# Kernel optimization log

Hardware: AMD Instinct MI355X
Metric: run time of the kernel (lower is better)

Reference implementation:

```python
import jax, jax.numpy as jnp
import numpy as np

HEAD_NUM = 8
NEG = 10000.0


def setup_inputs() -> dict:
    key = jax.random.key(0)
    ks = jax.random.split(key, 8)
    B, S, D = 2, 2048, 512
    sc = 1.0 / np.sqrt(D)
    return {
        "x": jax.random.normal(ks[0], (B, S, D), dtype=jnp.float32),
        "mask": jax.random.randint(ks[1], (B, S), 0, 2, dtype=jnp.int32),
        "Wq": jax.random.normal(ks[2], (D, D), dtype=jnp.float32) * sc,
        "bq": jnp.zeros((D,), jnp.float32),
        "Wk": jax.random.normal(ks[3], (D, D), dtype=jnp.float32) * sc,
        "bk": jnp.zeros((D,), jnp.float32),
        "Wv": jax.random.normal(ks[4], (D, D), dtype=jnp.float32) * sc,
        "bv": jnp.zeros((D,), jnp.float32),
        "Wo": jax.random.normal(ks[5], (D, D), dtype=jnp.float32) * sc,
        "bo": jnp.zeros((D,), jnp.float32),
    }


def _split_heads(t, H):
    B, S, D = t.shape
    return t.reshape(B, S, H, D // H).transpose(0, 2, 1, 3)  # [B,H,S,hd]


def reference(x, mask, Wq, bq, Wk, bk, Wv, bv, Wo, bo):
    B, S, D = x.shape
    H = HEAD_NUM
    hd = D // H
    # linear projections + relu activation (as in keras layer)
    q = jax.nn.relu(x @ Wq + bq)
    k = jax.nn.relu(x @ Wk + bk)
    v = jax.nn.relu(x @ Wv + bv)
    q = _split_heads(q, H)
    k = _split_heads(k, H)
    v = _split_heads(v, H)
    # scaled dot-product scores: scale by sqrt(head_dim) (query last dim after split)
    e = jnp.einsum("bhqd,bhkd->bhqk", q, k) / jnp.sqrt(jnp.float32(hd))
    # causal (history_only) additive mask
    idx = jnp.arange(S)
    causal = (idx[None, :] > idx[:, None]).astype(jnp.float32)  # [S,S]
    e = e - NEG * causal[None, None, :, :]
    # key padding mask, additive
    e = e - NEG * (1.0 - mask.astype(jnp.float32))[:, None, None, :]
    # stable softmax (explicit max-subtract as in source)
    a = jax.nn.softmax(e, axis=-1)
    out = jnp.einsum("bhqk,bhkd->bhqd", a, v)  # [B,H,S,hd]
    out = out.transpose(0, 2, 1, 3).reshape(B, S, D)
    # output projection + activation
    return jax.nn.relu(out @ Wo + bo)
```

## Files before the change

### kernel.cpp

```cpp
#include <hip/hip_runtime.h>
#include <hip/hip_bf16.h>

constexpr int Bc = 2, Sc = 2048, Dc = 512, Hc = 8, HDc = 64;
constexpr float NEGC = 10000.0f;
constexpr float SCALEC = 0.125f;
constexpr int Mtot = Bc * Sc;
constexpr size_t HEADMAT = (size_t)Bc * Hc * Sc * HDc;

typedef __attribute__((ext_vector_type(8))) short          short8;
typedef __attribute__((ext_vector_type(8))) unsigned short ushort8;
typedef __attribute__((ext_vector_type(4))) float          f32x4;

static __device__ __forceinline__ unsigned short f32_to_bf16_bits(float f) {
    unsigned int u = __builtin_bit_cast(unsigned int, f);
    unsigned int r = u + 0x7FFFu + ((u >> 16) & 1u);
    return (unsigned short)(r >> 16);
}

__global__ __launch_bounds__(256)
void convert_x(const float* __restrict__ x, unsigned short* __restrict__ Xb, int n)
{
    const int i = (blockIdx.x * 256 + threadIdx.x) * 4;
    if (i >= n) return;
    const float4 v = *(const float4*)(x + i);
    ushort4 o;
    o.x = f32_to_bf16_bits(v.x);
    o.y = f32_to_bf16_bits(v.y);
    o.z = f32_to_bf16_bits(v.z);
    o.w = f32_to_bf16_bits(v.w);
    *(ushort4*)(Xb + i) = o;
}

__global__ __launch_bounds__(256)
void transpose_w(const float* __restrict__ W0, const float* __restrict__ W1,
                 const float* __restrict__ W2, const float* __restrict__ W3,
                 unsigned short* __restrict__ Wt)
{
    __shared__ float T[64][65];
    const int z = blockIdx.z;
    const float* Wp = (z == 0) ? W0 : (z == 1) ? W1 : (z == 2) ? W2 : W3;
    unsigned short* Op = Wt + (size_t)z * 512 * 512;

    const int kt = blockIdx.y * 64, nt = blockIdx.x * 64;
    const int t = threadIdx.x;
    const int r  = t >> 2, c4 = (t & 3) * 16;

    #pragma unroll
    for (int i = 0; i < 4; ++i) {
        const float4 v = *(const float4*)(Wp + (size_t)(kt + r) * 512 + nt + c4 + 4 * i);
        T[r][c4 + 4*i + 0] = v.x;
        T[r][c4 + 4*i + 1] = v.y;
        T[r][c4 + 4*i + 2] = v.z;
        T[r][c4 + 4*i + 3] = v.w;
    }
    __syncthreads();

    const int n = t >> 2, k4 = (t & 3) * 16;
    #pragma unroll
    for (int i = 0; i < 4; ++i) {
        ushort4 o;
        o.x = f32_to_bf16_bits(T[k4 + 4*i + 0][n]);
        o.y = f32_to_bf16_bits(T[k4 + 4*i + 1][n]);
        o.z = f32_to_bf16_bits(T[k4 + 4*i + 2][n]);
        o.w = f32_to_bf16_bits(T[k4 + 4*i + 3][n]);
        *(ushort4*)(Op + (size_t)(nt + n) * 512 + kt + k4 + 4 * i) = o;
    }
}

template<bool HEADOUT>
__global__ __launch_bounds__(256)
void gemm_tile(const unsigned short* __restrict__ Xb,
               const unsigned short* __restrict__ Wt,
               const float* __restrict__ b0, const float* __restrict__ b1,
               const float* __restrict__ b2,
               unsigned short* __restrict__ Hout,
               float* __restrict__ Yf)
{
    __shared__ short As[128 * 32];
    __shared__ short Bs[64 * 32];

    const int lane = threadIdx.x & 63, wave = threadIdx.x >> 6;
    const int c = lane & 15, g = lane >> 4;
    const int wr = wave >> 1, wc = wave & 1;
    const int z = blockIdx.z;
    const unsigned short* Wp = Wt + (size_t)z * 512 * 512;
    const float* bp = (z == 0) ? b0 : (z == 1) ? b1 : b2;
    const int bm = blockIdx.y * 128;
    const int bn = blockIdx.x * 64;

    const int srow = lane >> 2;
    const int scol = (lane & 3) * 8;

    f32x4 acc[4][2] = {};

    for (int k0 = 0; k0 < 512; k0 += 32) {
        __syncthreads();
        #pragma unroll
        for (int i = 0; i < 2; ++i) {
            const int row = (wave * 2 + i) * 16 + srow;
            const short8 v = *(const short8*)(Xb + (size_t)(bm + row) * 512 + k0 + scol);
            *(short8*)(&As[row * 32 + scol]) = v;
        }
        {
            const int row = wave * 16 + srow;
            const short8 v = *(const short8*)(Wp + (size_t)(bn + row) * 512 + k0 + scol);
            *(short8*)(&Bs[row * 32 + scol]) = v;
        }
        __syncthreads();

        short8 a[4], b[2];
        #pragma unroll
        for (int mi = 0; mi < 4; ++mi)
            a[mi] = *(const short8*)(&As[(wr * 64 + mi * 16 + c) * 32 + g * 8]);
        #pragma unroll
        for (int ni = 0; ni < 2; ++ni)
            b[ni] = *(const short8*)(&Bs[(wc * 32 + ni * 16 + c) * 32 + g * 8]);
        #pragma unroll
        for (int mi = 0; mi < 4; ++mi)
            #pragma unroll
            for (int ni = 0; ni < 2; ++ni)
                acc[mi][ni] = __builtin_amdgcn_mfma_f32_16x16x32_bf16(
                    a[mi], b[ni], acc[mi][ni], 0, 0, 0);
    }

    #pragma unroll
    for (int mi = 0; mi < 4; ++mi) {
        #pragma unroll
        for (int ni = 0; ni < 2; ++ni) {
            const int n = bn + wc * 32 + ni * 16 + c;
            const float bias = bp[n];
            float v[4];
            #pragma unroll
            for (int r = 0; r < 4; ++r)
                v[r] = fmaxf(acc[mi][ni][r] + bias, 0.0f);
            const int mbase = bm + wr * 64 + mi * 16 + 4 * g;
            if constexpr (HEADOUT) {
                const int bb = mbase >> 11, ss = mbase & 2047;
                const int hh = n >> 6, hd = n & 63;
                #pragma unroll
                for (int r = 0; r < 4; ++r)
                    Hout[(size_t)z * HEADMAT +
                         (((size_t)(bb * Hc + hh) * Sc + ss + r) * HDc + hd)] =
                        f32_to_bf16_bits(v[r]);
            } else {
                #pragma unroll
                for (int r = 0; r < 4; ++r)
                    Yf[(size_t)(mbase + r) * 512 + n] = v[r];
            }
        }
    }
}

__global__ __launch_bounds__(256)
void attn_mfma(const short* __restrict__ Qh, const short* __restrict__ Kh,
               const short* __restrict__ Vh, const int* __restrict__ mask,
               unsigned short* __restrict__ Ob)
{
    __shared__ __align__(16) char smem[4 * 4608];

    const int lane = threadIdx.x & 63;
    const int wave = threadIdx.x >> 6;
    const int bid = blockIdx.x;
    const int swz = (bid & 7) * 256 + (bid >> 3);
    const int qt  = swz & 127;
    const int h   = (swz >> 7) & 7;
    const int b   = swz >> 10;
    const int q0  = qt * 16;
    const int c   = lane & 15;
    const int g   = lane >> 4;

    short* vst      = (short*)(smem + wave * 4608);
    float* LaccMine = (float*)(smem + wave * 4608);
    float* LmlMine  = (float*)(smem + wave * 4608 + 4352);

    const size_t headoff = (size_t)(b * Hc + h) * Sc * HDc;
    const short* Qp = Qh + headoff;
    const short* Kp = Kh + headoff;
    const short* Vp = Vh + headoff;
    const int* mb = mask + b * Sc;

    int fb = Sc;
    for (int base = 0; base < Sc; base += 64) {
        unsigned long long bal = __ballot(mb[base + lane] != 0);
        if (bal) { fb = base + (__ffsll((unsigned long long)bal) - 1); break; }
    }
    const int kmax = (fb <= q0) ? (q0 + 16) : Sc;
    const int kend = (kmax + 31) & ~31;

    const int nT   = kend >> 5;
    const int tpw  = (nT + 3) >> 2;
    const int kbeg = wave * tpw * 32;
    const int kfin = min(kend, kbeg + tpw * 32);

    const short8 qf0 = *(const short8*)(Qp + (size_t)(q0 + c) * HDc + g * 8);
    const short8 qf1 = *(const short8*)(Qp + (size_t)(q0 + c) * HDc + 32 + g * 8);

    f32x4 acc[4] = {{0.f,0.f,0.f,0.f},{0.f,0.f,0.f,0.f},
                    {0.f,0.f,0.f,0.f},{0.f,0.f,0.f,0.f}};
    float m = -1e30f, l = 0.0f;

    const int vrow = lane >> 1;
    const int vcol = (lane & 1) * 32;

    for (int k0 = kbeg; k0 < kfin; k0 += 32) {
        const short* vsrc = Vp + (size_t)(k0 + vrow) * HDc + vcol;
        const ushort8 vr0 = *(const ushort8*)(vsrc + 0);
        const ushort8 vr1 = *(const ushort8*)(vsrc + 8);
        const ushort8 vr2 = *(const ushort8*)(vsrc + 16);
        const ushort8 vr3 = *(const ushort8*)(vsrc + 24);

        const short8 kf0a = *(const short8*)(Kp + (size_t)(k0 + c) * HDc + g * 8);
        const short8 kf0b = *(const short8*)(Kp + (size_t)(k0 + c) * HDc + 32 + g * 8);
        const short8 kf1a = *(const short8*)(Kp + (size_t)(k0 + 16 + c) * HDc + g * 8);
        const short8 kf1b = *(const short8*)(Kp + (size_t)(k0 + 16 + c) * HDc + 32 + g * 8);

        f32x4 s0 = {0.f, 0.f, 0.f, 0.f};
        f32x4 s1 = {0.f, 0.f, 0.f, 0.f};
        s0 = __builtin_amdgcn_mfma_f32_16x16x32_bf16(kf0a, qf0, s0, 0, 0, 0);
        s0 = __builtin_amdgcn_mfma_f32_16x16x32_bf16(kf0b, qf1, s0, 0, 0, 0);
        s1 = __builtin_amdgcn_mfma_f32_16x16x32_bf16(kf1a, qf0, s1, 0, 0, 0);
        s1 = __builtin_amdgcn_mfma_f32_16x16x32_bf16(kf1b, qf1, s1, 0, 0, 0);

        const int4 mka = *(const int4*)(mb + k0 + 4 * g);
        const int4 mkb = *(const int4*)(mb + k0 + 16 + 4 * g);
        const int mia[4] = {mka.x, mka.y, mka.z, mka.w};
        const int mib[4] = {mkb.x, mkb.y, mkb.z, mkb.w};

        float e[8];
        float tmax = -1e30f;
        #pragma unroll
        for (int r = 0; r < 4; ++r) {
            const int keya = k0 + 4 * g + r;
            float ea = s0[r] * SCALEC;
            if (keya > q0 + c) ea -= NEGC;
            if (mia[r] == 0)   ea -= NEGC;
            e[r] = ea;
            const int keyb = k0 + 16 + 4 * g + r;
            float eb = s1[r] * SCALEC;
            if (keyb > q0 + c) eb -= NEGC;
            if (mib[r] == 0)   eb -= NEGC;
            e[4 + r] = eb;
            tmax = fmaxf(tmax, fmaxf(ea, eb));
        }
        tmax = fmaxf(tmax, __shfl_xor(tmax, 16));
        tmax = fmaxf(tmax, __shfl_xor(tmax, 32));

        if (__any(tmax > m)) {
            const float mnew = fmaxf(m, tmax);
            const float corr = __expf(m - mnew);
            m = mnew;
            l *= corr;
            float cq[4];
            #pragma unroll
            for (int r = 0; r < 4; ++r) cq[r] = __shfl(corr, 4 * g + r);
            #pragma unroll
            for (int t = 0; t < 4; ++t)
                #pragma unroll
                for (int r = 0; r < 4; ++r) acc[t][r] *= cq[r];
        }

        float p[8], ps = 0.f;
        #pragma unroll
        for (int j = 0; j < 8; ++j) { p[j] = __expf(e[j] - m); ps += p[j]; }
        l += ps;

        short8 pf;
        #pragma unroll
        for (int j = 0; j < 8; ++j) pf[j] = (short)f32_to_bf16_bits(p[j]);

        short* vdst = vst + vrow * 72 + vcol;
        *(ushort8*)(vdst + 0)  = vr0;
        *(ushort8*)(vdst + 8)  = vr1;
        *(ushort8*)(vdst + 16) = vr2;
        *(ushort8*)(vdst + 24) = vr3;

        #pragma unroll
        for (int t = 0; t < 4; ++t) {
            short8 vf;
            #pragma unroll
            for (int j = 0; j < 4; ++j) {
                vf[j]     = vst[(4 * g + j) * 72      + t * 16 + c];
                vf[4 + j] = vst[(16 + 4 * g + j) * 72 + t * 16 + c];
            }
            acc[t] = __builtin_amdgcn_mfma_f32_16x16x32_bf16(pf, vf, acc[t], 0, 0, 0);
        }
    }

    l = l + __shfl_xor(l, 16);
    l = l + __shfl_xor(l, 32);

    if (g == 0) { LmlMine[c] = m; LmlMine[16 + c] = l; }
    #pragma unroll
    for (int t = 0; t < 4; ++t)
        #pragma unroll
        for (int r = 0; r < 4; ++r)
            LaccMine[(4 * g + r) * 68 + t * 16 + c] = acc[t][r];
    __syncthreads();

    const int col = wave * 16 + c;
    #pragma unroll
    for (int r = 0; r < 4; ++r) {
        const int row = 4 * g + r;
        float mu[4], lu[4], ou[4];
        #pragma unroll
        for (int u = 0; u < 4; ++u) {
            const float* LaccU = (const float*)(smem + u * 4608);
            const float* LmlU  = (const float*)(smem + u * 4608 + 4352);
            mu[u] = LmlU[row];
            lu[u] = LmlU[16 + row];
            ou[u] = LaccU[row * 68 + col];
        }
        const float M = fmaxf(fmaxf(mu[0], mu[1]), fmaxf(mu[2], mu[3]));
        float L = 0.f, o = 0.f;
        #pragma unroll
        for (int u = 0; u < 4; ++u) {
            const float w = __expf(mu[u] - M);
            L += w * lu[u];
            o += w * ou[u];
        }
        Ob[(size_t)(b * Sc + q0 + row) * Dc + h * HDc + col] =
            f32_to_bf16_bits(o / L);
    }
}

extern "C" void kernel_launch(void* const* d_in, const int* in_sizes, int n_in,
                              void* d_out, int out_size, void* d_ws, size_t ws_size,
                              hipStream_t stream) {
    const float* x  = (const float*)d_in[0];
    const int* mask = (const int*)d_in[1];
    const float* Wq = (const float*)d_in[2];
    const float* bq = (const float*)d_in[3];
    const float* Wk = (const float*)d_in[4];
    const float* bk = (const float*)d_in[5];
    const float* Wv = (const float*)d_in[6];
    const float* bv = (const float*)d_in[7];
    const float* Wo = (const float*)d_in[8];
    const float* bo = (const float*)d_in[9];
    float* out = (float*)d_out;

    unsigned short* Xb = (unsigned short*)d_ws;
    unsigned short* Wt = Xb + (size_t)Mtot * 512;
    unsigned short* Qh = Wt + (size_t)4 * 512 * 512;
    unsigned short* Kh = Qh + HEADMAT;
    unsigned short* Vh = Kh + HEADMAT;
    unsigned short* Ob = Vh + HEADMAT;

    convert_x<<<dim3((Mtot * 512) / 1024), dim3(256), 0, stream>>>(
        x, Xb, Mtot * 512);
    transpose_w<<<dim3(8, 8, 4), dim3(256), 0, stream>>>(Wq, Wk, Wv, Wo, Wt);
    gemm_tile<true><<<dim3(8, Mtot / 128, 3), dim3(256), 0, stream>>>(
        Xb, Wt, bq, bk, bv, Qh, nullptr);
    attn_mfma<<<dim3(2048), dim3(256), 0, stream>>>(
        (const short*)Qh, (const short*)Kh, (const short*)Vh, mask, Ob);
    gemm_tile<false><<<dim3(8, Mtot / 128, 1), dim3(256), 0, stream>>>(
        Ob, Wt + (size_t)3 * 512 * 512, bo, bo, bo, nullptr, out);
}
```

Baseline: 108.6 us.

## Process 32 queries per attention block to reuse K/V tiles, use exp2

The attention kernel now handles two 16-row query tiles per block, so each K and V tile loaded from global memory and staged in LDS feeds twice as many MFMAs. The grid is halved, shared memory per wave doubles, and register use rises with the second set of accumulators. Softmax is rewritten in base 2 with prescaled constants, so exp2 replaces expf. The causal comparison is skipped for key tiles that lie entirely before the query tile. Fewer blocks and higher register pressure may reduce occupancy and latency hiding.

Result: no change. 109.7 us (+1.0%).

```diff
diff --git a/kernel.cpp b/kernel.cpp
--- a/kernel.cpp
+++ b/kernel.cpp
@@ -2,14 +2,16 @@
 #include <hip/hip_bf16.h>
 
 constexpr int Bc = 2, Sc = 2048, Dc = 512, Hc = 8, HDc = 64;
-constexpr float NEGC = 10000.0f;
-constexpr float SCALEC = 0.125f;
 constexpr int Mtot = Bc * Sc;
 constexpr size_t HEADMAT = (size_t)Bc * Hc * Sc * HDc;
+constexpr float SC2  = 0.18033688011112042f;
+constexpr float NEG2 = 14426.950408889634f;
 
 typedef __attribute__((ext_vector_type(8))) short          short8;
 typedef __attribute__((ext_vector_type(8))) unsigned short ushort8;
 typedef __attribute__((ext_vector_type(4))) float          f32x4;
+
+#define MFMA16 __builtin_amdgcn_mfma_f32_16x16x32_bf16
 
 static __device__ __forceinline__ unsigned short f32_to_bf16_bits(float f) {
     unsigned int u = __builtin_bit_cast(unsigned int, f);
@@ -108,19 +110,18 @@
         }
         __syncthreads();
 
-        short8 a[4], b[2];
+        short8 a[4], bfr[2];
         #pragma unroll
         for (int mi = 0; mi < 4; ++mi)
             a[mi] = *(const short8*)(&As[(wr * 64 + mi * 16 + c) * 32 + g * 8]);
         #pragma unroll
         for (int ni = 0; ni < 2; ++ni)
-            b[ni] = *(const short8*)(&Bs[(wc * 32 + ni * 16 + c) * 32 + g * 8]);
+            bfr[ni] = *(const short8*)(&Bs[(wc * 32 + ni * 16 + c) * 32 + g * 8]);
         #pragma unroll
         for (int mi = 0; mi < 4; ++mi)
             #pragma unroll
             for (int ni = 0; ni < 2; ++ni)
-                acc[mi][ni] = __builtin_amdgcn_mfma_f32_16x16x32_bf16(
-                    a[mi], b[ni], acc[mi][ni], 0, 0, 0);
+                acc[mi][ni] = MFMA16(a[mi], bfr[ni], acc[mi][ni], 0, 0, 0);
     }
 
     #pragma unroll
@@ -156,22 +157,23 @@
                const short* __restrict__ Vh, const int* __restrict__ mask,
                unsigned short* __restrict__ Ob)
 {
-    __shared__ __align__(16) char smem[4 * 4608];
+    __shared__ __align__(16) char smem[4 * 9216];
 
     const int lane = threadIdx.x & 63;
     const int wave = threadIdx.x >> 6;
-    const int bid = blockIdx.x;
-    const int swz = (bid & 7) * 256 + (bid >> 3);
-    const int qt  = swz & 127;
-    const int h   = (swz >> 7) & 7;
-    const int b   = swz >> 10;
-    const int q0  = qt * 16;
-    const int c   = lane & 15;
-    const int g   = lane >> 4;
-
-    short* vst      = (short*)(smem + wave * 4608);
-    float* LaccMine = (float*)(smem + wave * 4608);
-    float* LmlMine  = (float*)(smem + wave * 4608 + 4352);
+    const int bid  = blockIdx.x;
+    const int swz  = (bid & 7) * 128 + (bid >> 3);
+    const int qt   = swz & 63;
+    const int h    = (swz >> 6) & 7;
+    const int b    = swz >> 9;
+    const int q0   = qt * 32;
+    const int c    = lane & 15;
+    const int g    = lane >> 4;
+
+    char*  wbase = smem + wave * 9216;
+    short* vst   = (short*)wbase;
+    float* Lacc  = (float*)wbase;
+    float* Lml   = (float*)(wbase + 8704);
 
     const size_t headoff = (size_t)(b * Hc + h) * Sc * HDc;
     const short* Qp = Qh + headoff;
@@ -182,22 +184,23 @@
     int fb = Sc;
     for (int base = 0; base < Sc; base += 64) {
         unsigned long long bal = __ballot(mb[base + lane] != 0);
-        if (bal) { fb = base + (__ffsll((unsigned long long)bal) - 1); break; }
-    }
-    const int kmax = (fb <= q0) ? (q0 + 16) : Sc;
+        if (bal) { fb = base + (__ffsll(bal) - 1); break; }
+    }
+    const int kmax = (fb <= q0) ? (q0 + 32) : Sc;
     const int kend = (kmax + 31) & ~31;
-
     const int nT   = kend >> 5;
     const int tpw  = (nT + 3) >> 2;
     const int kbeg = wave * tpw * 32;
     const int kfin = min(kend, kbeg + tpw * 32);
 
-    const short8 qf0 = *(const short8*)(Qp + (size_t)(q0 + c) * HDc + g * 8);
-    const short8 qf1 = *(const short8*)(Qp + (size_t)(q0 + c) * HDc + 32 + g * 8);
-
-    f32x4 acc[4] = {{0.f,0.f,0.f,0.f},{0.f,0.f,0.f,0.f},
-                    {0.f,0.f,0.f,0.f},{0.f,0.f,0.f,0.f}};
-    float m = -1e30f, l = 0.0f;
+    const short8 qa0 = *(const short8*)(Qp + (size_t)(q0 + c) * HDc + g * 8);
+    const short8 qa1 = *(const short8*)(Qp + (size_t)(q0 + c) * HDc + 32 + g * 8);
+    const short8 qb0 = *(const short8*)(Qp + (size_t)(q0 + 16 + c) * HDc + g * 8);
+    const short8 qb1 = *(const short8*)(Qp + (size_t)(q0 + 16 + c) * HDc + 32 + g * 8);
+
+    f32x4 accA[4] = {{0,0,0,0},{0,0,0,0},{0,0,0,0},{0,0,0,0}};
+    f32x4 accB[4] = {{0,0,0,0},{0,0,0,0},{0,0,0,0},{0,0,0,0}};
+    float mA = -1e30f, lA = 0.f, mB = -1e30f, lB = 0.f;
 
     const int vrow = lane >> 1;
     const int vcol = (lane & 1) * 32;
@@ -214,59 +217,95 @@
         const short8 kf1a = *(const short8*)(Kp + (size_t)(k0 + 16 + c) * HDc + g * 8);
         const short8 kf1b = *(const short8*)(Kp + (size_t)(k0 + 16 + c) * HDc + 32 + g * 8);
 
-        f32x4 s0 = {0.f, 0.f, 0.f, 0.f};
-        f32x4 s1 = {0.f, 0.f, 0.f, 0.f};
-        s0 = __builtin_amdgcn_mfma_f32_16x16x32_bf16(kf0a, qf0, s0, 0, 0, 0);
-        s0 = __builtin_amdgcn_mfma_f32_16x16x32_bf16(kf0b, qf1, s0, 0, 0, 0);
-        s1 = __builtin_amdgcn_mfma_f32_16x16x32_bf16(kf1a, qf0, s1, 0, 0, 0);
-        s1 = __builtin_amdgcn_mfma_f32_16x16x32_bf16(kf1b, qf1, s1, 0, 0, 0);
+        f32x4 sa0 = {0,0,0,0}, sa1 = {0,0,0,0};
+        f32x4 sb0 = {0,0,0,0}, sb1 = {0,0,0,0};
+        sa0 = MFMA16(kf0a, qa0, sa0, 0, 0, 0);
+        sa0 = MFMA16(kf0b, qa1, sa0, 0, 0, 0);
+        sa1 = MFMA16(kf1a, qa0, sa1, 0, 0, 0);
+        sa1 = MFMA16(kf1b, qa1, sa1, 0, 0, 0);
+        sb0 = MFMA16(kf0a, qb0, sb0, 0, 0, 0);
+        sb0 = MFMA16(kf0b, qb1, sb0, 0, 0, 0);
+        sb1 = MFMA16(kf1a, qb0, sb1, 0, 0, 0);
+        sb1 = MFMA16(kf1b, qb1, sb1, 0, 0, 0);
 
         const int4 mka = *(const int4*)(mb + k0 + 4 * g);
         const int4 mkb = *(const int4*)(mb + k0 + 16 + 4 * g);
         const int mia[4] = {mka.x, mka.y, mka.z, mka.w};
         const int mib[4] = {mkb.x, mkb.y, mkb.z, mkb.w};
 
-        float e[8];
-        float tmax = -1e30f;
-        #pragma unroll
-        for (int r = 0; r < 4; ++r) {
-            const int keya = k0 + 4 * g + r;
-            float ea = s0[r] * SCALEC;
-            if (keya > q0 + c) ea -= NEGC;
-            if (mia[r] == 0)   ea -= NEGC;
-            e[r] = ea;
-            const int keyb = k0 + 16 + 4 * g + r;
-            float eb = s1[r] * SCALEC;
-            if (keyb > q0 + c) eb -= NEGC;
-            if (mib[r] == 0)   eb -= NEGC;
-            e[4 + r] = eb;
-            tmax = fmaxf(tmax, fmaxf(ea, eb));
-        }
-        tmax = fmaxf(tmax, __shfl_xor(tmax, 16));
-        tmax = fmaxf(tmax, __shfl_xor(tmax, 32));
-
-        if (__any(tmax > m)) {
-            const float mnew = fmaxf(m, tmax);
-            const float corr = __expf(m - mnew);
-            m = mnew;
-            l *= corr;
+        float eA[8], eB[8];
+        float tA = -1e30f, tB = -1e30f;
+        if (k0 + 31 > q0) {
+            #pragma unroll
+            for (int r = 0; r < 4; ++r) {
+                const int ka = k0 + 4 * g + r;
+                const int kb = k0 + 16 + 4 * g + r;
+                float e0 = sa0[r] * SC2; if (ka > q0 + c)      e0 -= NEG2;
+                float e1 = sa1[r] * SC2; if (kb > q0 + c)      e1 -= NEG2;
+                float e2 = sb0[r] * SC2; if (ka > q0 + 16 + c) e2 -= NEG2;
+                float e3 = sb1[r] * SC2; if (kb > q0 + 16 + c) e3 -= NEG2;
+                if (mia[r] == 0) { e0 -= NEG2; e2 -= NEG2; }
+                if (mib[r] == 0) { e1 -= NEG2; e3 -= NEG2; }
+                eA[r] = e0; eA[4 + r] = e1; tA = fmaxf(tA, fmaxf(e0, e1));
+                eB[r] = e2; eB[4 + r] = e3; tB = fmaxf(tB, fmaxf(e2, e3));
+            }
+        } else {
+            #pragma unroll
+            for (int r = 0; r < 4; ++r) {
+                float e0 = sa0[r] * SC2;
+                float e1 = sa1[r] * SC2;
+                float e2 = sb0[r] * SC2;
+                float e3 = sb1[r] * SC2;
+                if (mia[r] == 0) { e0 -= NEG2; e2 -= NEG2; }
+                if (mib[r] == 0) { e1 -= NEG2; e3 -= NEG2; }
+                eA[r] = e0; eA[4 + r] = e1; tA = fmaxf(tA, fmaxf(e0, e1));
+                eB[r] = e2; eB[4 + r] = e3; tB = fmaxf(tB, fmaxf(e2, e3));
+            }
+        }
+        tA = fmaxf(tA, __shfl_xor(tA, 16));
+        tB = fmaxf(tB, __shfl_xor(tB, 16));
+        tA = fmaxf(tA, __shfl_xor(tA, 32));
+        tB = fmaxf(tB, __shfl_xor(tB, 32));
+
+        if (__any(tA > mA)) {
+            const float mn = fmaxf(mA, tA);
+            const float corr = __builtin_exp2f(mA - mn);
+            mA = mn; lA *= corr;
             float cq[4];
             #pragma unroll
             for (int r = 0; r < 4; ++r) cq[r] = __shfl(corr, 4 * g + r);
             #pragma unroll
             for (int t = 0; t < 4; ++t)
                 #pragma unroll
-                for (int r = 0; r < 4; ++r) acc[t][r] *= cq[r];
-        }
-
-        float p[8], ps = 0.f;
-        #pragma unroll
-        for (int j = 0; j < 8; ++j) { p[j] = __expf(e[j] - m); ps += p[j]; }
-        l += ps;
-
-        short8 pf;
-        #pragma unroll
-        for (int j = 0; j < 8; ++j) pf[j] = (short)f32_to_bf16_bits(p[j]);
+                for (int r = 0; r < 4; ++r) accA[t][r] *= cq[r];
+        }
+        if (__any(tB > mB)) {
+            const float mn = fmaxf(mB, tB);
+            const float corr = __builtin_exp2f(mB - mn);
+            mB = mn; lB *= corr;
+            float cq[4];
+            #pragma unroll
+            for (int r = 0; r < 4; ++r) cq[r] = __shfl(corr, 4 * g + r);
+            #pragma unroll
+            for (int t = 0; t < 4; ++t)
+                #pragma unroll
+                for (int r = 0; r < 4; ++r) accB[t][r] *= cq[r];
+        }
+
+        float pA[8], pB[8], psA = 0.f, psB = 0.f;
+        #pragma unroll
+        for (int j = 0; j < 8; ++j) {
+            pA[j] = __builtin_exp2f(eA[j] - mA); psA += pA[j];
+            pB[j] = __builtin_exp2f(eB[j] - mB); psB += pB[j];
+        }
+        lA += psA; lB += psB;
+
+        short8 pfa, pfb;
+        #pragma unroll
+        for (int j = 0; j < 8; ++j) {
+            pfa[j] = (short)f32_to_bf16_bits(pA[j]);
+            pfb[j] = (short)f32_to_bf16_bits(pB[j]);
+        }
 
         short* vdst = vst + vrow * 72 + vcol;
         *(ushort8*)(vdst + 0)  = vr0;
@@ -282,45 +321,53 @@
                 vf[j]     = vst[(4 * g + j) * 72      + t * 16 + c];
                 vf[4 + j] = vst[(16 + 4 * g + j) * 72 + t * 16 + c];
             }
-            acc[t] = __builtin_amdgcn_mfma_f32_16x16x32_bf16(pf, vf, acc[t], 0, 0, 0);
-        }
-    }
-
-    l = l + __shfl_xor(l, 16);
-    l = l + __shfl_xor(l, 32);
-
-    if (g == 0) { LmlMine[c] = m; LmlMine[16 + c] = l; }
+            accA[t] = MFMA16(pfa, vf, accA[t], 0, 0, 0);
+            accB[t] = MFMA16(pfb, vf, accB[t], 0, 0, 0);
+        }
+    }
+
+    lA += __shfl_xor(lA, 16); lA += __shfl_xor(lA, 32);
+    lB += __shfl_xor(lB, 16); lB += __shfl_xor(lB, 32);
+
+    if (g == 0) {
+        Lml[c]      = mA;  Lml[16 + c] = mB;
+        Lml[32 + c] = lA;  Lml[48 + c] = lB;
+    }
     #pragma unroll
     for (int t = 0; t < 4; ++t)
         #pragma unroll
-        for (int r = 0; r < 4; ++r)
-            LaccMine[(4 * g + r) * 68 + t * 16 + c] = acc[t][r];
+        for (int r = 0; r < 4; ++r) {
+            Lacc[(4 * g + r) * 68 + t * 16 + c]      = accA[t][r];
+            Lacc[(16 + 4 * g + r) * 68 + t * 16 + c] = accB[t][r];
+        }
     __syncthreads();
 
     const int col = wave * 16 + c;
     #pragma unroll
-    for (int r = 0; r < 4; ++r) {
-        const int row = 4 * g + r;
-        float mu[4], lu[4], ou[4];
-        #pragma unroll
-        for (int u = 0; u < 4; ++u) {
-            const float* LaccU = (const float*)(smem + u * 4608);
-            const float* LmlU  = (const float*)(smem + u * 4608 + 4352);
-            mu[u] = LmlU[row];
-            lu[u] = LmlU[16 + row];
-            ou[u] = LaccU[row * 68 + col];
-        }
-        const float M = fmaxf(fmaxf(mu[0], mu[1]), fmaxf(mu[2], mu[3]));
-        float L = 0.f, o = 0.f;
-        #pragma unroll
-        for (int u = 0; u < 4; ++u) {
-            const float w = __expf(mu[u] - M);
-            L += w * lu[u];
-            o += w * ou[u];
-        }
-        Ob[(size_t)(b * Sc + q0 + row) * Dc + h * HDc + col] =
-            f32_to_bf16_bits(o / L);
-    }
+    for (int half = 0; half < 2; ++half)
+        #pragma unroll
+        for (int r = 0; r < 4; ++r) {
+            const int row = half * 16 + 4 * g + r;
+            float mu[4], lu[4], ou[4], M = -1e30f;
+            #pragma unroll
+            for (int u = 0; u < 4; ++u) {
+                const float* LaccU = (const float*)(smem + u * 9216);
+                const float* LmlU  = (const float*)(smem + u * 9216 + 8704);
+                mu[u] = LmlU[row];
+                lu[u] = LmlU[32 + row];
+                ou[u] = LaccU[row * 68 + col];
+                M = fmaxf(M, mu[u]);
+            }
+            float L = 0.f, o = 0.f;
+            #pragma unroll
+            for (int u = 0; u < 4; ++u) {
+                const float w = __builtin_exp2f(mu[u] - M);
+                L += w * lu[u];
+                o += w * ou[u];
+            }
+            Ob[(size_t)(b * Sc + q0 + row) * Dc + h * HDc + col] =
+                f32_to_bf16_bits(o / L);
+        }
 }
 
 extern "C" void kernel_launch(void* const* d_in, const int* in_sizes, int n_in,
@@ -350,7 +397,7 @@
     transpose_w<<<dim3(8, 8, 4), dim3(256), 0, stream>>>(Wq, Wk, Wv, Wo, Wt);
     gemm_tile<true><<<dim3(8, Mtot / 128, 3), dim3(256), 0, stream>>>(
         Xb, Wt, bq, bk, bv, Qh, nullptr);
-    attn_mfma<<<dim3(2048), dim3(256), 0, stream>>>(
+    attn_mfma<<<dim3(1024), dim3(256), 0, stream>>>(
         (const short*)Qh, (const short*)Kh, (const short*)Vh, mask, Ob);
     gemm_tile<false><<<dim3(8, Mtot / 128, 1), dim3(256), 0, stream>>>(
         Ob, Wt + (size_t)3 * 512 * 512, bo, bo, bo, nullptr, out);
```

## Use 32x32 MFMA with 32-query tiles and exp2 softmax in attention

Applied to the files above, without the earlier changes.

Reworks the attention kernel so each block handles 32 queries with 32x32x16 bf16 MFMAs instead of 16 queries with 16x16 MFMAs, halving the grid and doubling K/V reuse per load. Switches softmax to exp2 with scale and mask constants prefolded by log2(e), builds the key mask from a wave ballot, and skips the causal compare for tiles fully below the diagonal. Probabilities are repacked across lane halves with shuffles to form the B operand, and the cross-wave merge is redone with a larger padded LDS buffer. This cuts redundant K/V traffic and per-element work, at the cost of more registers, more LDS per block, and fewer blocks to fill the GPU.

After: 95.98 us. 11.6% less time.

```diff
diff --git a/kernel.cpp b/kernel.cpp
--- a/kernel.cpp
+++ b/kernel.cpp
@@ -2,19 +2,27 @@
 #include <hip/hip_bf16.h>
 
 constexpr int Bc = 2, Sc = 2048, Dc = 512, Hc = 8, HDc = 64;
-constexpr float NEGC = 10000.0f;
-constexpr float SCALEC = 0.125f;
 constexpr int Mtot = Bc * Sc;
 constexpr size_t HEADMAT = (size_t)Bc * Hc * Sc * HDc;
-
-typedef __attribute__((ext_vector_type(8))) short          short8;
-typedef __attribute__((ext_vector_type(8))) unsigned short ushort8;
-typedef __attribute__((ext_vector_type(4))) float          f32x4;
+constexpr float SC2  = 0.18033688011112042f;
+constexpr float NEG2 = 14426.950408889634f;
+
+typedef __attribute__((ext_vector_type(8)))  short          short8;
+typedef __attribute__((ext_vector_type(8)))  unsigned short ushort8;
+typedef __attribute__((ext_vector_type(4)))  float          f32x4;
+typedef __attribute__((ext_vector_type(16))) float          f32x16;
+
+#define MFMA16 __builtin_amdgcn_mfma_f32_16x16x32_bf16
+#define MFMA32 __builtin_amdgcn_mfma_f32_32x32x16_bf16
 
 static __device__ __forceinline__ unsigned short f32_to_bf16_bits(float f) {
     unsigned int u = __builtin_bit_cast(unsigned int, f);
     unsigned int r = u + 0x7FFFu + ((u >> 16) & 1u);
     return (unsigned short)(r >> 16);
+}
+static __device__ __forceinline__ unsigned int pkbf(float a, float b) {
+    return (unsigned int)f32_to_bf16_bits(a) |
+           ((unsigned int)f32_to_bf16_bits(b) << 16);
 }
 
 __global__ __launch_bounds__(256)
@@ -108,19 +116,18 @@
         }
         __syncthreads();
 
-        short8 a[4], b[2];
+        short8 a[4], bfr[2];
         #pragma unroll
         for (int mi = 0; mi < 4; ++mi)
             a[mi] = *(const short8*)(&As[(wr * 64 + mi * 16 + c) * 32 + g * 8]);
         #pragma unroll
         for (int ni = 0; ni < 2; ++ni)
-            b[ni] = *(const short8*)(&Bs[(wc * 32 + ni * 16 + c) * 32 + g * 8]);
+            bfr[ni] = *(const short8*)(&Bs[(wc * 32 + ni * 16 + c) * 32 + g * 8]);
         #pragma unroll
         for (int mi = 0; mi < 4; ++mi)
             #pragma unroll
             for (int ni = 0; ni < 2; ++ni)
-                acc[mi][ni] = __builtin_amdgcn_mfma_f32_16x16x32_bf16(
-                    a[mi], b[ni], acc[mi][ni], 0, 0, 0);
+                acc[mi][ni] = MFMA16(a[mi], bfr[ni], acc[mi][ni], 0, 0, 0);
     }
 
     #pragma unroll
@@ -156,22 +163,22 @@
                const short* __restrict__ Vh, const int* __restrict__ mask,
                unsigned short* __restrict__ Ob)
 {
-    __shared__ __align__(16) char smem[4 * 4608];
+    __shared__ __align__(16) char smem[4 * 8448 + 4 * 256];
 
     const int lane = threadIdx.x & 63;
     const int wave = threadIdx.x >> 6;
-    const int bid = blockIdx.x;
-    const int swz = (bid & 7) * 256 + (bid >> 3);
-    const int qt  = swz & 127;
-    const int h   = (swz >> 7) & 7;
-    const int b   = swz >> 10;
-    const int q0  = qt * 16;
-    const int c   = lane & 15;
-    const int g   = lane >> 4;
-
-    short* vst      = (short*)(smem + wave * 4608);
-    float* LaccMine = (float*)(smem + wave * 4608);
-    float* LmlMine  = (float*)(smem + wave * 4608 + 4352);
+    const int bid  = blockIdx.x;
+    const int swz  = (bid & 7) * 128 + (bid >> 3);
+    const int t    = swz & 63;
+    const int h    = (swz >> 6) & 7;
+    const int b    = swz >> 9;
+    const int q0   = t * 32;
+    const int r32  = lane & 31;
+    const int hi   = lane >> 5;
+
+    char*  wreg = smem + wave * 8448;
+    short* vst  = (short*)wreg;
+    float* Lml  = (float*)(smem + 4 * 8448 + wave * 256);
 
     const size_t headoff = (size_t)(b * Hc + h) * Sc * HDc;
     const short* Qp = Qh + headoff;
@@ -182,25 +189,25 @@
     int fb = Sc;
     for (int base = 0; base < Sc; base += 64) {
         unsigned long long bal = __ballot(mb[base + lane] != 0);
-        if (bal) { fb = base + (__ffsll((unsigned long long)bal) - 1); break; }
-    }
-    const int kmax = (fb <= q0) ? (q0 + 16) : Sc;
+        if (bal) { fb = base + (__ffsll(bal) - 1); break; }
+    }
+    const int kmax = (fb <= q0) ? (q0 + 32) : Sc;
     const int kend = (kmax + 31) & ~31;
-
     const int nT   = kend >> 5;
     const int tpw  = (nT + 3) >> 2;
     const int kbeg = wave * tpw * 32;
     const int kfin = min(kend, kbeg + tpw * 32);
 
-    const short8 qf0 = *(const short8*)(Qp + (size_t)(q0 + c) * HDc + g * 8);
-    const short8 qf1 = *(const short8*)(Qp + (size_t)(q0 + c) * HDc + 32 + g * 8);
-
-    f32x4 acc[4] = {{0.f,0.f,0.f,0.f},{0.f,0.f,0.f,0.f},
-                    {0.f,0.f,0.f,0.f},{0.f,0.f,0.f,0.f}};
+    short8 qf[4];
+    #pragma unroll
+    for (int j = 0; j < 4; ++j)
+        qf[j] = *(const short8*)(Qp + (size_t)(q0 + r32) * HDc + j * 16 + hi * 8);
+
+    f32x16 acc0 = {0,0,0,0,0,0,0,0,0,0,0,0,0,0,0,0};
+    f32x16 acc1 = {0,0,0,0,0,0,0,0,0,0,0,0,0,0,0,0};
     float m = -1e30f, l = 0.0f;
 
-    const int vrow = lane >> 1;
-    const int vcol = (lane & 1) * 32;
+    const int vrow = lane >> 1, vcol = (lane & 1) * 32;
 
     for (int k0 = kbeg; k0 < kfin; k0 += 32) {
         const short* vsrc = Vp + (size_t)(k0 + vrow) * HDc + vcol;
@@ -209,64 +216,75 @@
         const ushort8 vr2 = *(const ushort8*)(vsrc + 16);
         const ushort8 vr3 = *(const ushort8*)(vsrc + 24);
 
-        const short8 kf0a = *(const short8*)(Kp + (size_t)(k0 + c) * HDc + g * 8);
-        const short8 kf0b = *(const short8*)(Kp + (size_t)(k0 + c) * HDc + 32 + g * 8);
-        const short8 kf1a = *(const short8*)(Kp + (size_t)(k0 + 16 + c) * HDc + g * 8);
-        const short8 kf1b = *(const short8*)(Kp + (size_t)(k0 + 16 + c) * HDc + 32 + g * 8);
-
-        f32x4 s0 = {0.f, 0.f, 0.f, 0.f};
-        f32x4 s1 = {0.f, 0.f, 0.f, 0.f};
-        s0 = __builtin_amdgcn_mfma_f32_16x16x32_bf16(kf0a, qf0, s0, 0, 0, 0);
-        s0 = __builtin_amdgcn_mfma_f32_16x16x32_bf16(kf0b, qf1, s0, 0, 0, 0);
-        s1 = __builtin_amdgcn_mfma_f32_16x16x32_bf16(kf1a, qf0, s1, 0, 0, 0);
-        s1 = __builtin_amdgcn_mfma_f32_16x16x32_bf16(kf1b, qf1, s1, 0, 0, 0);
-
-        const int4 mka = *(const int4*)(mb + k0 + 4 * g);
-        const int4 mkb = *(const int4*)(mb + k0 + 16 + 4 * g);
-        const int mia[4] = {mka.x, mka.y, mka.z, mka.w};
-        const int mib[4] = {mkb.x, mkb.y, mkb.z, mkb.w};
-
-        float e[8];
+        f32x16 s = {0,0,0,0,0,0,0,0,0,0,0,0,0,0,0,0};
+        #pragma unroll
+        for (int j = 0; j < 4; ++j) {
+            const short8 kf =
+                *(const short8*)(Kp + (size_t)(k0 + r32) * HDc + j * 16 + hi * 8);
+            s = MFMA32(kf, qf[j], s, 0, 0, 0);
+        }
+
+        const unsigned long long bal = __ballot(mb[k0 + r32] != 0);
+        const unsigned int mloc = ((unsigned int)bal) >> (4 * hi);
+
+        float e[16];
         float tmax = -1e30f;
-        #pragma unroll
-        for (int r = 0; r < 4; ++r) {
-            const int keya = k0 + 4 * g + r;
-            float ea = s0[r] * SCALEC;
-            if (keya > q0 + c) ea -= NEGC;
-            if (mia[r] == 0)   ea -= NEGC;
-            e[r] = ea;
-            const int keyb = k0 + 16 + 4 * g + r;
-            float eb = s1[r] * SCALEC;
-            if (keyb > q0 + c) eb -= NEGC;
-            if (mib[r] == 0)   eb -= NEGC;
-            e[4 + r] = eb;
-            tmax = fmaxf(tmax, fmaxf(ea, eb));
-        }
-        tmax = fmaxf(tmax, __shfl_xor(tmax, 16));
+        if (k0 + 31 > q0) {
+            #pragma unroll
+            for (int r = 0; r < 16; ++r) {
+                const int cr0 = (r & 3) + 8 * (r >> 2);
+                float ev = s[r] * SC2;
+                if (!((mloc >> cr0) & 1))            ev -= NEG2;
+                if (k0 + cr0 + 4 * hi > q0 + r32)    ev -= NEG2;
+                e[r] = ev;
+                tmax = fmaxf(tmax, ev);
+            }
+        } else {
+            #pragma unroll
+            for (int r = 0; r < 16; ++r) {
+                const int cr0 = (r & 3) + 8 * (r >> 2);
+                float ev = s[r] * SC2;
+                if (!((mloc >> cr0) & 1))            ev -= NEG2;
+                e[r] = ev;
+                tmax = fmaxf(tmax, ev);
+            }
+        }
         tmax = fmaxf(tmax, __shfl_xor(tmax, 32));
 
         if (__any(tmax > m)) {
-            const float mnew = fmaxf(m, tmax);
-            const float corr = __expf(m - mnew);
-            m = mnew;
-            l *= corr;
-            float cq[4];
-            #pragma unroll
-            for (int r = 0; r < 4; ++r) cq[r] = __shfl(corr, 4 * g + r);
-            #pragma unroll
-            for (int t = 0; t < 4; ++t)
-                #pragma unroll
-                for (int r = 0; r < 4; ++r) acc[t][r] *= cq[r];
-        }
-
-        float p[8], ps = 0.f;
-        #pragma unroll
-        for (int j = 0; j < 8; ++j) { p[j] = __expf(e[j] - m); ps += p[j]; }
+            const float mn   = fmaxf(m, tmax);
+            const float corr = __builtin_exp2f(m - mn);
+            m = mn; l *= corr;
+            acc0 *= corr;
+            acc1 *= corr;
+        }
+
+        float ps = 0.f;
+        #pragma unroll
+        for (int r = 0; r < 16; ++r) {
+            e[r] = __builtin_exp2f(e[r] - m);
+            ps += e[r];
+        }
         l += ps;
 
-        short8 pf;
-        #pragma unroll
-        for (int j = 0; j < 8; ++j) pf[j] = (short)f32_to_bf16_bits(p[j]);
+        const unsigned int A0 = pkbf(e[0],  e[1]),  B0 = pkbf(e[2],  e[3]);
+        const unsigned int C0 = pkbf(e[4],  e[5]),  D0 = pkbf(e[6],  e[7]);
+        const unsigned int A1 = pkbf(e[8],  e[9]),  B1 = pkbf(e[10], e[11]);
+        const unsigned int C1 = pkbf(e[12], e[13]), D1 = pkbf(e[14], e[15]);
+        const unsigned int A0s = (unsigned int)__shfl_xor((int)A0, 32);
+        const unsigned int B0s = (unsigned int)__shfl_xor((int)B0, 32);
+        const unsigned int C0s = (unsigned int)__shfl_xor((int)C0, 32);
+        const unsigned int D0s = (unsigned int)__shfl_xor((int)D0, 32);
+        const unsigned int A1s = (unsigned int)__shfl_xor((int)A1, 32);
+        const unsigned int B1s = (unsigned int)__shfl_xor((int)B1, 32);
+        const unsigned int C1s = (unsigned int)__shfl_xor((int)C1, 32);
+        const unsigned int D1s = (unsigned int)__shfl_xor((int)D1, 32);
+
+        union { unsigned int u[4]; short8 s8; } P0, P1;
+        P0.u[0] = hi ? C0s : A0;  P0.u[1] = hi ? D0s : B0;
+        P0.u[2] = hi ? C0  : A0s; P0.u[3] = hi ? D0  : B0s;
+        P1.u[0] = hi ? C1s : A1;  P1.u[1] = hi ? D1s : B1;
+        P1.u[2] = hi ? C1  : A1s; P1.u[3] = hi ? D1  : B1s;
 
         short* vdst = vst + vrow * 72 + vcol;
         *(ushort8*)(vdst + 0)  = vr0;
@@ -274,52 +292,65 @@
         *(ushort8*)(vdst + 16) = vr2;
         *(ushort8*)(vdst + 24) = vr3;
 
-        #pragma unroll
-        for (int t = 0; t < 4; ++t) {
-            short8 vf;
-            #pragma unroll
-            for (int j = 0; j < 4; ++j) {
-                vf[j]     = vst[(4 * g + j) * 72      + t * 16 + c];
-                vf[4 + j] = vst[(16 + 4 * g + j) * 72 + t * 16 + c];
-            }
-            acc[t] = __builtin_amdgcn_mfma_f32_16x16x32_bf16(pf, vf, acc[t], 0, 0, 0);
-        }
-    }
-
-    l = l + __shfl_xor(l, 16);
-    l = l + __shfl_xor(l, 32);
-
-    if (g == 0) { LmlMine[c] = m; LmlMine[16 + c] = l; }
-    #pragma unroll
-    for (int t = 0; t < 4; ++t)
-        #pragma unroll
-        for (int r = 0; r < 4; ++r)
-            LaccMine[(4 * g + r) * 68 + t * 16 + c] = acc[t][r];
+        short8 va;
+        #pragma unroll
+        for (int e8 = 0; e8 < 8; ++e8)
+            va[e8] = vst[(8 * hi + e8) * 72 + r32];
+        acc0 = MFMA32(va, P0.s8, acc0, 0, 0, 0);
+        #pragma unroll
+        for (int e8 = 0; e8 < 8; ++e8)
+            va[e8] = vst[(16 + 8 * hi + e8) * 72 + r32];
+        acc0 = MFMA32(va, P1.s8, acc0, 0, 0, 0);
+        #pragma unroll
+        for (int e8 = 0; e8 < 8; ++e8)
+            va[e8] = vst[(8 * hi + e8) * 72 + 32 + r32];
+        acc1 = MFMA32(va, P0.s8, acc1, 0, 0, 0);
+        #pragma unroll
+        for (int e8 = 0; e8 < 8; ++e8)
+            va[e8] = vst[(16 + 8 * hi + e8) * 72 + 32 + r32];
+        acc1 = MFMA32(va, P1.s8, acc1, 0, 0, 0);
+    }
+
+    l += __shfl_xor(l, 32);
+
+    {
+        float* Lacc = (float*)wreg;
+        #pragma unroll
+        for (int r = 0; r < 16; ++r) {
+            Lacc[lane * 33 + r]      = acc0[r];
+            Lacc[lane * 33 + 16 + r] = acc1[r];
+        }
+        if (lane < 32) { Lml[lane] = m; Lml[32 + lane] = l; }
+    }
     __syncthreads();
 
-    const int col = wave * 16 + c;
-    #pragma unroll
-    for (int r = 0; r < 4; ++r) {
-        const int row = 4 * g + r;
-        float mu[4], lu[4], ou[4];
-        #pragma unroll
-        for (int u = 0; u < 4; ++u) {
-            const float* LaccU = (const float*)(smem + u * 4608);
-            const float* LmlU  = (const float*)(smem + u * 4608 + 4352);
-            mu[u] = LmlU[row];
-            lu[u] = LmlU[16 + row];
-            ou[u] = LaccU[row * 68 + col];
-        }
-        const float M = fmaxf(fmaxf(mu[0], mu[1]), fmaxf(mu[2], mu[3]));
-        float L = 0.f, o = 0.f;
-        #pragma unroll
-        for (int u = 0; u < 4; ++u) {
-            const float w = __expf(mu[u] - M);
-            L += w * lu[u];
-            o += w * ou[u];
-        }
-        Ob[(size_t)(b * Sc + q0 + row) * Dc + h * HDc + col] =
-            f32_to_bf16_bits(o / L);
+    float mu[4], lu[4], M = -1e30f;
+    #pragma unroll
+    for (int u = 0; u < 4; ++u) {
+        const float* LmlU = (const float*)(smem + 4 * 8448 + u * 256);
+        mu[u] = LmlU[r32];
+        lu[u] = LmlU[32 + r32];
+        M = fmaxf(M, mu[u]);
+    }
+    float wgt[4], L = 0.f;
+    #pragma unroll
+    for (int u = 0; u < 4; ++u) {
+        wgt[u] = __builtin_exp2f(mu[u] - M);
+        L += wgt[u] * lu[u];
+    }
+    const float invL = 1.0f / L;
+
+    #pragma unroll
+    for (int jj = 0; jj < 8; ++jj) {
+        const int j = wave * 8 + jj;
+        float o = 0.f;
+        #pragma unroll
+        for (int u = 0; u < 4; ++u)
+            o += wgt[u] * ((const float*)(smem + u * 8448))[lane * 33 + j];
+        const int j16 = j & 15;
+        const int d = (j16 & 3) + 8 * (j16 >> 2) + 4 * hi + 32 * (j >> 4);
+        Ob[(size_t)(b * Sc + q0 + r32) * Dc + h * HDc + d] =
+            f32_to_bf16_bits(o * invL);
     }
 }
 
@@ -350,7 +381,7 @@
     transpose_w<<<dim3(8, 8, 4), dim3(256), 0, stream>>>(Wq, Wk, Wv, Wo, Wt);
     gemm_tile<true><<<dim3(8, Mtot / 128, 3), dim3(256), 0, stream>>>(
         Xb, Wt, bq, bk, bv, Qh, nullptr);
-    attn_mfma<<<dim3(2048), dim3(256), 0, stream>>>(
+    attn_mfma<<<dim3(1024), dim3(256), 0, stream>>>(
         (const short*)Qh, (const short*)Kh, (const short*)Vh, mask, Ob);
     gemm_tile<false><<<dim3(8, Mtot / 128, 1), dim3(256), 0, stream>>>(
         Ob, Wt + (size_t)3 * 512 * 512, bo, bo, bo, nullptr, out);
```
